# Kernel optimization log

Hardware: AMD Instinct MI355X
Metric: run time of the kernel (lower is better)

The kernel has to match this reference:

```python
import jax, jax.numpy as jnp
import numpy as np

N_SRC, N_DST, N_EDGES = 200000, 100000, 600000
D_IN, D_OUT = 128, 128
NUM_EDGE_TYPES = 7
SCALING_FACTOR = 100.0


def setup_inputs() -> dict:
    key = jax.random.key(0)
    ks = jax.random.split(key, 6)
    x_src = jax.random.normal(ks[0], (N_SRC, D_IN), dtype=jnp.float32)
    x_target = jax.random.normal(ks[1], (N_DST, D_IN), dtype=jnp.float32)
    row = jax.random.randint(ks[2], (N_EDGES,), 0, N_SRC, dtype=jnp.int64 if jax.config.jax_enable_x64 else jnp.int32)
    col = jax.random.randint(ks[3], (N_EDGES,), 0, N_DST, dtype=jnp.int64 if jax.config.jax_enable_x64 else jnp.int32)
    edge_type = jax.random.randint(ks[4], (N_EDGES,), 0, NUM_EDGE_TYPES, dtype=jnp.int32)
    # Parameters (mirroring reset_parameters): xavier_uniform weight, zero bias,
    # relation_weight = 1/scaling_factor constant.
    limit = float(np.sqrt(6.0 / (D_IN + D_OUT)))
    weight = jax.random.uniform(ks[5], (D_IN, D_OUT), minval=-limit, maxval=limit, dtype=jnp.float32)
    bias = jnp.zeros((D_OUT,), dtype=jnp.float32)
    relation_weight = jnp.full((NUM_EDGE_TYPES,), 1.0 / SCALING_FACTOR, dtype=jnp.float32)
    return {"x_src": x_src, "x_target": x_target, "row": row, "col": col,
            "edge_type": edge_type, "weight": weight, "bias": bias,
            "relation_weight": relation_weight}


def reference(x_src, x_target, row, col, edge_type, weight, bias, relation_weight):
    n_dst = x_target.shape[0]
    # per-type linear transform (shared weight, applied to src and target)
    h_src = x_src @ weight                      # [N_src, D_out]
    h_tgt = x_target @ weight                   # [N_dst, D_out] (computed as in original; unused by 'add' aggr)
    # relation weights: one-hot(e_feat) @ leaky_relu(rw * s) == gather
    rw = jax.nn.leaky_relu(relation_weight * SCALING_FACTOR)
    edge_weight = rw[edge_type]                 # [E]
    # weighted in-degree normalization over destination nodes
    deg = jax.ops.segment_sum(edge_weight, col, num_segments=n_dst)  # [N_dst]
    ew = edge_weight / deg[col]                 # [E]
    # gather -> scale -> scatter-add message passing
    msg = ew[:, None] * h_src[row]              # [E, D_out]
    out = jnp.zeros((n_dst, h_src.shape[1]), dtype=h_src.dtype).at[col].add(msg)
    return out + bias
```

## Files before the change

kernel.cpp:

```cpp
#include <hip/hip_runtime.h>

#define D 128
#define CAP 64

typedef __attribute__((ext_vector_type(8))) short bf16x8;
typedef __attribute__((ext_vector_type(4))) float f32x4;
typedef __attribute__((ext_vector_type(8))) ushort ushort8;

struct EW { int r; float w; };

__device__ __forceinline__ float rel_w(const float* __restrict__ rel, int t) {
    float v = rel[t] * 100.0f;
    return v > 0.0f ? v : 0.01f * v;
}

__device__ __forceinline__ ushort f2b(float x) {
    unsigned u = __float_as_uint(x);
    u += 0x7FFFu + ((u >> 16) & 1u);
    return (ushort)(u >> 16);
}

__device__ __forceinline__ float b2f(ushort u) {
    return __uint_as_float((unsigned)u << 16);
}


__global__ void k_init(int* __restrict__ cnt, const float* __restrict__ W,
                       ushort* __restrict__ Wt, int ndst) {
    const int i = blockIdx.x * blockDim.x + threadIdx.x;
    if (i < ndst) cnt[i] = 0;
    if (i < D * D) {
        const int n = i >> 7, k = i & 127;
        Wt[i] = f2b(W[k * D + n]);
    }
}

__global__ __launch_bounds__(512, 6) void k_fused(const float* __restrict__ X,
                                                  const ushort* __restrict__ Wt,
                                                  ushort* __restrict__ Hb, int nrows,
                                                  const int* __restrict__ col,
                                                  const int* __restrict__ row,
                                                  const int* __restrict__ et,
                                                  const float* __restrict__ rel,
                                                  int* __restrict__ cnt,
                                                  EW* __restrict__ ewr, int ne, int nbg) {
    __shared__ ushort sW[D * 136];
    const int t = threadIdx.x;

    if (blockIdx.x >= nbg) {
        const int e = (blockIdx.x - nbg) * blockDim.x + t;
        if (e < ne) {
            const int c = col[e];
            const int p = atomicAdd(&cnt[c], 1);
            if (p < CAP) {
                EW rec; rec.r = row[e]; rec.w = rel_w(rel, et[e]);
                ewr[(size_t)c * CAP + p] = rec;
            }
        }
        return;
    }

    #pragma unroll
    for (int p = 0; p < 4; ++p) {
        const int idx = p * 4096 + t * 8;
        const int n = idx >> 7, k = idx & 127;
        *(bf16x8*)&sW[n * 136 + k] = *(const bf16x8*)&Wt[idx];
    }
    __syncthreads();

    const int rbase = blockIdx.x * 128;
    const int w = t >> 6, l = t & 63;
    const int m16 = l & 15, g4 = l >> 4;
    const int arow = rbase + w * 16 + m16;
    const bool valid = (arow < nrows);
    const size_t xoff = (size_t)(valid ? arow : 0) * D;

    f32x4 acc[8] = {};
    #pragma unroll
    for (int ks = 0; ks < 4; ++ks) {
        const int k0 = ks * 32 + g4 * 8;
        const float4 xa = *(const float4*)&X[xoff + k0];
        const float4 xb = *(const float4*)&X[xoff + k0 + 4];
        union { ushort us[8]; bf16x8 v; } a;
        a.us[0] = f2b(xa.x); a.us[1] = f2b(xa.y); a.us[2] = f2b(xa.z); a.us[3] = f2b(xa.w);
        a.us[4] = f2b(xb.x); a.us[5] = f2b(xb.y); a.us[6] = f2b(xb.z); a.us[7] = f2b(xb.w);
        #pragma unroll
        for (int nf = 0; nf < 8; ++nf) {
            const bf16x8 b = *(const bf16x8*)&sW[(nf * 16 + m16) * 136 + k0];
            acc[nf] = __builtin_amdgcn_mfma_f32_16x16x32_bf16(a.v, b, acc[nf], 0, 0, 0);
        }
    }

    #pragma unroll
    for (int q = 0; q < 4; ++q) {
        const int r = rbase + w * 16 + g4 * 4 + q;
        if (r < nrows) {
            ushort8 o;
            #pragma unroll
            for (int nf = 0; nf < 8; ++nf) o[nf] = f2b(acc[nf][q]);
            *(ushort8*)&Hb[(size_t)r * D + m16 * 8] = o;
        }
    }
}

__global__ __launch_bounds__(256) void k_agg(const ushort* __restrict__ Hb,
                                             const EW* __restrict__ ewr,
                                             const int* __restrict__ cnt,
                                             const float* __restrict__ bias,
                                             float* __restrict__ out, int ndst) {
    const int dw = (int)((blockIdx.x * blockDim.x + threadIdx.x) >> 6);
    const int lane = threadIdx.x & 63;
    if (dw >= ndst) return;
    const int c = min(cnt[dw], CAP);
    const int m16 = lane & 15, g4 = lane >> 4;

    EW e0; e0.r = 0; e0.w = 0.f;
    if (lane < c) e0 = ewr[(size_t)dw * CAP + lane];

    float wsum = e0.w;
    #pragma unroll
    for (int s = 1; s < 64; s <<= 1) wsum += __shfl_xor(wsum, s);
    const float inv = (wsum != 0.f) ? 1.f / wsum : 0.f;

    const int r0 = e0.r; const float wv = e0.w * inv;
    float acc[8] = {};
    for (int j0 = 0; j0 < c; j0 += 4) {
        const int j = j0 + g4;
        const int   rr = __shfl(r0, j);
        const float ww = __shfl(wv, j);
        const ushort8 hv = *(const ushort8*)&Hb[(size_t)rr * D + m16 * 8];
        #pragma unroll
        for (int i = 0; i < 8; ++i)
            acc[i] = fmaf(ww, b2f(hv[i]), acc[i]);
    }

    #pragma unroll
    for (int i = 0; i < 8; ++i) {
        acc[i] += __shfl_xor(acc[i], 16);
        acc[i] += __shfl_xor(acc[i], 32);
    }

    if (lane < 16) {
        #pragma unroll
        for (int i = 0; i < 8; ++i) {
            const int cj = i * 16 + m16;
            out[(size_t)dw * D + cj] = acc[i] + bias[cj];
        }
    }
}

extern "C" void kernel_launch(void* const* d_in, const int* in_sizes, int n_in,
                              void* d_out, int out_size, void* d_ws, size_t ws_size,
                              hipStream_t stream) {
    const float* x_src  = (const float*)d_in[0];
    const int*   row    = (const int*)d_in[2];
    const int*   col    = (const int*)d_in[3];
    const int*   etype  = (const int*)d_in[4];
    const float* weight = (const float*)d_in[5];
    const float* bias   = (const float*)d_in[6];
    const float* relw   = (const float*)d_in[7];

    const int nsrc = in_sizes[0] / D;
    const int ndst = out_size / D;
    const int ne   = in_sizes[2];

    ushort* Hb  = (ushort*)d_ws;
    ushort* Wt  = Hb + (size_t)nsrc * D;
    EW*     ewr = (EW*)(Wt + D * D);
    int*    cnt = (int*)(ewr + (size_t)ndst * CAP);

    float* out = (float*)d_out;

    const int nbg = (nsrc + 127) / 128;
    const int nbe = (ne + 511) / 512;
    const int ninit = max(ndst, D * D);

    hipLaunchKernelGGL(k_init, dim3((ninit + 255) / 256), dim3(256), 0, stream,
                       cnt, weight, Wt, ndst);
    hipLaunchKernelGGL(k_fused, dim3(nbg + nbe), dim3(512), 0, stream,
                       x_src, Wt, Hb, nsrc, col, row, etype, relw, cnt, ewr, ne, nbg);
    hipLaunchKernelGGL(k_agg, dim3((ndst + 3) / 4), dim3(256), 0, stream,
                       Hb, ewr, cnt, bias, out, ndst);
}
```

Baseline: 101.9 us.

## Drop init kernel, convert weight in-block, and loop GEMM blocks over two tiles

Removes the separate init kernel. The counter array is now cleared with hipMemsetAsync, and each GEMM block transposes and converts the fp32 weight to bf16 into shared memory itself. The GEMM grid is halved, so each block walks two row tiles and the per-block weight staging is amortised over them. This trades one kernel launch and the Wt workspace pass for strided, uncoalesced fp32 weight reads in every block and fewer GEMM blocks running alongside the edge-bucketing blocks.

```diff
diff --git a/kernel.cpp b/kernel.cpp
--- a/kernel.cpp
+++ b/kernel.cpp
@@ -25,25 +25,16 @@
 }
 
 
-__global__ void k_init(int* __restrict__ cnt, const float* __restrict__ W,
-                       ushort* __restrict__ Wt, int ndst) {
-    const int i = blockIdx.x * blockDim.x + threadIdx.x;
-    if (i < ndst) cnt[i] = 0;
-    if (i < D * D) {
-        const int n = i >> 7, k = i & 127;
-        Wt[i] = f2b(W[k * D + n]);
-    }
-}
-
 __global__ __launch_bounds__(512, 6) void k_fused(const float* __restrict__ X,
-                                                  const ushort* __restrict__ Wt,
+                                                  const float* __restrict__ W,
                                                   ushort* __restrict__ Hb, int nrows,
                                                   const int* __restrict__ col,
                                                   const int* __restrict__ row,
                                                   const int* __restrict__ et,
                                                   const float* __restrict__ rel,
                                                   int* __restrict__ cnt,
-                                                  EW* __restrict__ ewr, int ne, int nbg) {
+                                                  EW* __restrict__ ewr, int ne,
+                                                  int nbg, int ntiles) {
     __shared__ ushort sW[D * 136];
     const int t = threadIdx.x;
 
@@ -64,41 +55,49 @@
     for (int p = 0; p < 4; ++p) {
         const int idx = p * 4096 + t * 8;
         const int n = idx >> 7, k = idx & 127;
-        *(bf16x8*)&sW[n * 136 + k] = *(const bf16x8*)&Wt[idx];
+        ushort8 v;
+        #pragma unroll
+        for (int j = 0; j < 8; ++j) v[j] = f2b(W[(size_t)(k + j) * D + n]);
+        *(ushort8*)&sW[n * 136 + k] = v;
     }
     __syncthreads();
 
-    const int rbase = blockIdx.x * 128;
     const int w = t >> 6, l = t & 63;
     const int m16 = l & 15, g4 = l >> 4;
-    const int arow = rbase + w * 16 + m16;
-    const bool valid = (arow < nrows);
-    const size_t xoff = (size_t)(valid ? arow : 0) * D;
 
-    f32x4 acc[8] = {};
-    #pragma unroll
-    for (int ks = 0; ks < 4; ++ks) {
-        const int k0 = ks * 32 + g4 * 8;
-        const float4 xa = *(const float4*)&X[xoff + k0];
-        const float4 xb = *(const float4*)&X[xoff + k0 + 4];
-        union { ushort us[8]; bf16x8 v; } a;
-        a.us[0] = f2b(xa.x); a.us[1] = f2b(xa.y); a.us[2] = f2b(xa.z); a.us[3] = f2b(xa.w);
-        a.us[4] = f2b(xb.x); a.us[5] = f2b(xb.y); a.us[6] = f2b(xb.z); a.us[7] = f2b(xb.w);
+    for (int tb = blockIdx.x; tb < ntiles; tb += nbg) {
+        const int rbase = tb * 128;
+        const int arow = rbase + w * 16 + m16;
+        const bool valid = (arow < nrows);
+        const size_t xoff = (size_t)(valid ? arow : 0) * D;
+
+        f32x4 acc[8] = {};
         #pragma unroll
-        for (int nf = 0; nf < 8; ++nf) {
-            const bf16x8 b = *(const bf16x8*)&sW[(nf * 16 + m16) * 136 + k0];
-            acc[nf] = __builtin_amdgcn_mfma_f32_16x16x32_bf16(a.v, b, acc[nf], 0, 0, 0);
+        for (int ks = 0; ks < 4; ++ks) {
+            const int k0 = ks * 32 + g4 * 8;
+            const float4 xa = *(const float4*)&X[xoff + k0];
+            const float4 xb = *(const float4*)&X[xoff + k0 + 4];
+            union { ushort us[8]; bf16x8 v; } a;
+            a.us[0] = f2b(xa.x); a.us[1] = f2b(xa.y);
+            a.us[2] = f2b(xa.z); a.us[3] = f2b(xa.w);
+            a.us[4] = f2b(xb.x); a.us[5] = f2b(xb.y);
+            a.us[6] = f2b(xb.z); a.us[7] = f2b(xb.w);
+            #pragma unroll
+            for (int nf = 0; nf < 8; ++nf) {
+                const bf16x8 b = *(const bf16x8*)&sW[(nf * 16 + m16) * 136 + k0];
+                acc[nf] = __builtin_amdgcn_mfma_f32_16x16x32_bf16(a.v, b, acc[nf], 0, 0, 0);
+            }
         }
-    }
 
-    #pragma unroll
-    for (int q = 0; q < 4; ++q) {
-        const int r = rbase + w * 16 + g4 * 4 + q;
-        if (r < nrows) {
-            ushort8 o;
-            #pragma unroll
-            for (int nf = 0; nf < 8; ++nf) o[nf] = f2b(acc[nf][q]);
-            *(ushort8*)&Hb[(size_t)r * D + m16 * 8] = o;
+        #pragma unroll
+        for (int q = 0; q < 4; ++q) {
+            const int r = rbase + w * 16 + g4 * 4 + q;
+            if (r < nrows) {
+                ushort8 o;
+                #pragma unroll
+                for (int nf = 0; nf < 8; ++nf) o[nf] = f2b(acc[nf][q]);
+                *(ushort8*)&Hb[(size_t)r * D + m16 * 8] = o;
+            }
         }
     }
 }
@@ -165,20 +164,19 @@
     const int ne   = in_sizes[2];
 
     ushort* Hb  = (ushort*)d_ws;
-    ushort* Wt  = Hb + (size_t)nsrc * D;
-    EW*     ewr = (EW*)(Wt + D * D);
+    EW*     ewr = (EW*)(Hb + (size_t)nsrc * D);
     int*    cnt = (int*)(ewr + (size_t)ndst * CAP);
 
     float* out = (float*)d_out;
 
-    const int nbg = (nsrc + 127) / 128;
-    const int nbe = (ne + 511) / 512;
-    const int ninit = max(ndst, D * D);
+    const int ntiles = (nsrc + 127) / 128;
+    const int nbg    = (ntiles + 1) / 2;
+    const int nbe    = (ne + 511) / 512;
 
-    hipLaunchKernelGGL(k_init, dim3((ninit + 255) / 256), dim3(256), 0, stream,
-                       cnt, weight, Wt, ndst);
+    hipMemsetAsync(cnt, 0, (size_t)ndst * sizeof(int), stream);
     hipLaunchKernelGGL(k_fused, dim3(nbg + nbe), dim3(512), 0, stream,
-                       x_src, Wt, Hb, nsrc, col, row, etype, relw, cnt, ewr, ne, nbg);
+                       x_src, weight, Hb, nsrc, col, row, etype, relw, cnt, ewr, ne,
+                       nbg, ntiles);
     hipLaunchKernelGGL(k_agg, dim3((ndst + 3) / 4), dim3(256), 0, stream,
                        Hb, ewr, cnt, bias, out, ndst);
 }
```

New measurement: 222.9 us. +118.9%, slower.
